# Kernel optimization log

Measured on AMD Instinct MI355X. Metric: run time of the kernel, lower is better.

Reference implementation:

```python
import jax, jax.numpy as jnp
import numpy as np

N_LAYERS = 3
EMB_DIM = 64
N_MASHUP = 100000
N_API = 50000
N_EDGES_MASHUP = 3200000
N_EDGES_API = 1600000
EPS = 1e-12  # F.normalize clamp_min epsilon


def setup_inputs() -> dict:
    key = jax.random.key(0)
    ks = jax.random.split(key, 8)
    return {
        "adj_mashup_rows": jax.random.randint(ks[0], (N_EDGES_MASHUP,), 0, N_MASHUP, dtype=jnp.int32),
        "adj_mashup_cols": jax.random.randint(ks[1], (N_EDGES_MASHUP,), 0, N_MASHUP, dtype=jnp.int32),
        "adj_mashup_vals": jax.random.uniform(ks[2], (N_EDGES_MASHUP,), dtype=jnp.float32),
        "adj_api_rows": jax.random.randint(ks[3], (N_EDGES_API,), 0, N_API, dtype=jnp.int32),
        "adj_api_cols": jax.random.randint(ks[4], (N_EDGES_API,), 0, N_API, dtype=jnp.int32),
        "adj_api_vals": jax.random.uniform(ks[5], (N_EDGES_API,), dtype=jnp.float32),
        "mashup_emb": jax.random.normal(ks[6], (N_MASHUP, EMB_DIM), dtype=jnp.float32),
        "api_emb": jax.random.normal(ks[7], (N_API, EMB_DIM), dtype=jnp.float32),
    }


def _spmm(rows, cols, vals, x, n_nodes):
    # sparse [n,n] @ dense [n,d] via gather + weighted segment-sum
    return jax.ops.segment_sum(vals[:, None] * x[cols], rows, num_segments=n_nodes)


def _propagate(rows, cols, vals, emb):
    n = emb.shape[0]
    acc = emb
    cur = emb
    for _ in range(N_LAYERS):
        cur = _spmm(rows, cols, vals, cur, n)
        acc = acc + cur
    out = acc / (N_LAYERS + 1)  # mean over stacked layers (incl. layer 0)
    norm = jnp.maximum(jnp.linalg.norm(out, axis=1, keepdims=True), EPS)
    return out / norm


def reference(adj_mashup_rows, adj_mashup_cols, adj_mashup_vals,
              adj_api_rows, adj_api_cols, adj_api_vals,
              mashup_emb, api_emb):
    final_mashup = _propagate(adj_mashup_rows, adj_mashup_cols, adj_mashup_vals, mashup_emb)
    final_api = _propagate(adj_api_rows, adj_api_cols, adj_api_vals, api_emb)
    return final_mashup, final_api
```

## Files before the change

kernel.cpp:

```cpp
#include <hip/hip_runtime.h>


#define EMB_DIM 64
#define UNR 8
typedef unsigned long long ull;
typedef int v4i __attribute__((ext_vector_type(4)));

static inline int cdiv(long long a, long long b) { return (int)((a + b - 1) / b); }


__global__ void k_zero2(int* __restrict__ pm, int nm_, int* __restrict__ pa,
                        int na_) {
    int i = blockIdx.x * blockDim.x + threadIdx.x;
    if (i < nm_) pm[i] = 0;
    else if (i < nm_ + na_) pa[i - nm_] = 0;
}

__global__ void k_hist2(const int* __restrict__ rm, int nem,
                        int* __restrict__ posm, const int* __restrict__ ra,
                        int nea, int* __restrict__ posa) {
    int nm4 = nem >> 2, na4 = nea >> 2;
    int i = blockIdx.x * blockDim.x + threadIdx.x;
    if (i < nm4) {
        v4i r = __builtin_nontemporal_load((const v4i*)rm + i);
        atomicAdd(&posm[r.x], 1);
        atomicAdd(&posm[r.y], 1);
        atomicAdd(&posm[r.z], 1);
        atomicAdd(&posm[r.w], 1);
    } else if (i < nm4 + na4) {
        v4i r = __builtin_nontemporal_load((const v4i*)ra + (i - nm4));
        atomicAdd(&posa[r.x], 1);
        atomicAdd(&posa[r.y], 1);
        atomicAdd(&posa[r.z], 1);
        atomicAdd(&posa[r.w], 1);
    } else if (i == nm4 + na4) {
        for (int t = nm4 << 2; t < nem; ++t) atomicAdd(&posm[rm[t]], 1);
        for (int t = na4 << 2; t < nea; ++t) atomicAdd(&posa[ra[t]], 1);
    }
}

#define SCAN_B 256
#define SCAN_E 1024
__global__ void k_scan1(const int* __restrict__ in, int n,
                        int* __restrict__ out, int* __restrict__ bsums) {
    __shared__ int lds[SCAN_B];
    int t = threadIdx.x;
    int base = blockIdx.x * SCAN_E + t * 4;
    int v[4];
    int s = 0;
#pragma unroll
    for (int j = 0; j < 4; ++j) {
        v[j] = (base + j < n) ? in[base + j] : 0;
        s += v[j];
    }
    lds[t] = s;
    __syncthreads();
    for (int off = 1; off < SCAN_B; off <<= 1) {
        int x = (t >= off) ? lds[t - off] : 0;
        __syncthreads();
        lds[t] += x;
        __syncthreads();
    }
    int run = lds[t] - s;
    if (t == SCAN_B - 1) bsums[blockIdx.x] = lds[t];
#pragma unroll
    for (int j = 0; j < 4; ++j) {
        if (base + j < n) out[base + j] = run;
        run += v[j];
    }
}

__global__ void k_scan2(int* __restrict__ bsums, int nb) {
    __shared__ int lds[1024];
    int t = threadIdx.x;
    int v = (t < nb) ? bsums[t] : 0;
    lds[t] = v;
    __syncthreads();
    for (int off = 1; off < 1024; off <<= 1) {
        int x = (t >= off) ? lds[t - off] : 0;
        __syncthreads();
        lds[t] += x;
        __syncthreads();
    }
    if (t < nb) bsums[t] = lds[t] - v;
}

__global__ void k_scan3(int* __restrict__ row_ptr, int* __restrict__ row_pos,
                        const int* __restrict__ bsums, int n, int ne) {
    int i = blockIdx.x * blockDim.x + threadIdx.x;
    if (i < n) {
        int p = row_ptr[i] + bsums[i >> 10];
        row_ptr[i] = p;
        row_pos[i] = p;
    }
    if (i == 0) row_ptr[n] = ne;
}

__global__ void k_scatter2(const int* __restrict__ rm,
                           const int* __restrict__ cm,
                           const float* __restrict__ vm, int nem,
                           unsigned pmulm, int* __restrict__ posm,
                           ull* __restrict__ evm, const int* __restrict__ ra,
                           const int* __restrict__ ca,
                           const float* __restrict__ va, int nea,
                           unsigned pmula, int* __restrict__ posa,
                           ull* __restrict__ eva, int bm) {
    const int p = blockIdx.x & 7;
    const bool is_m = (int)blockIdx.x < bm;
    const int b = is_m ? blockIdx.x : blockIdx.x - bm;
    const int nslot = (is_m ? bm : (int)gridDim.x - bm) >> 3;
    const int bslot = b >> 3;

    const int* rows = is_m ? rm : ra;
    const int* cols = is_m ? cm : ca;
    const float* vals = is_m ? vm : va;
    const int ne = is_m ? nem : nea;
    const unsigned pmul = is_m ? pmulm : pmula;
    int* row_pos = is_m ? posm : posa;
    ull* ev = is_m ? evm : eva;

    const int nb4 = ne >> 2;
    const v4i* rows4 = (const v4i*)rows;

    for (int g = bslot * blockDim.x + threadIdx.x; g < nb4;
         g += nslot * blockDim.x) {
        v4i r4 = __builtin_nontemporal_load(rows4 + g);
        int base = g << 2;
#pragma unroll
        for (int k = 0; k < 4; ++k) {
            int r = (k == 0) ? r4.x : (k == 1) ? r4.y : (k == 2) ? r4.z : r4.w;
            if ((int)(((unsigned)r * pmul) >> 16) == p) {
                int i = base + k;
                float v = __builtin_nontemporal_load(vals + i);
                int c = __builtin_nontemporal_load(cols + i);
                ull pk = ((ull)__float_as_uint(v) << 32) | (unsigned)c;
                int pos = atomicAdd(&row_pos[r], 1);
                ev[pos] = pk;
            }
        }
    }
    if (bslot == 0 && threadIdx.x == 0) {
        for (int i = nb4 << 2; i < ne; ++i) {
            int r = rows[i];
            if ((int)(((unsigned)r * pmul) >> 16) == p) {
                ull pk = ((ull)__float_as_uint(vals[i]) << 32) |
                         (unsigned)cols[i];
                int pos = atomicAdd(&row_pos[r], 1);
                ev[pos] = pk;
            }
        }
    }
}


__global__ void k_tohalf(const float* __restrict__ s, _Float16* __restrict__ d,
                         int n) {
    int i = (blockIdx.x * blockDim.x + threadIdx.x) * 4;
    if (i < n) {
        float4 v = *reinterpret_cast<const float4*>(s + i);
        _Float16 h[4] = {(_Float16)v.x, (_Float16)v.y, (_Float16)v.z,
                         (_Float16)v.w};
        *reinterpret_cast<ushort4*>(d + i) = *reinterpret_cast<ushort4*>(h);
    }
}

template <bool FIRST, bool LAST>
__global__ void k_spmm_quad(const ull* __restrict__ ev,
                            const int* __restrict__ row_ptr,
                            const _Float16* __restrict__ x,
                            _Float16* __restrict__ nxt,
                            float* __restrict__ acc,
                            const float* __restrict__ emb, int nrows) {
    int row = (int)((blockIdx.x * blockDim.x + threadIdx.x) >> 6);
    if (row >= nrows) return;
    int lane = threadIdx.x & 63;
    int q = lane >> 4;
    int sub = lane & 15;

    int s = row_ptr[row];
    int cnt = row_ptr[row + 1] - s;
    const ull* evr = ev + s;

    float a0[UNR], a1[UNR], a2[UNR], a3[UNR];
#pragma unroll
    for (int k = 0; k < UNR; ++k) {
        a0[k] = 0.f; a1[k] = 0.f; a2[k] = 0.f; a3[k] = 0.f;
    }

    int j = 0;
    for (; j + 4 * UNR <= cnt; j += 4 * UNR) {
        ull p[UNR];
#pragma unroll
        for (int k = 0; k < UNR; ++k)
            p[k] = __builtin_nontemporal_load(evr + j + 4 * k + q);
#pragma unroll
        for (int k = 0; k < UNR; ++k) {
            unsigned c = (unsigned)p[k];
            ull xd = *reinterpret_cast<const ull*>(
                x + ((size_t)c << 6) + (sub << 2));
            float v = __uint_as_float((unsigned)(p[k] >> 32));
            union { ull u; _Float16 f[4]; } cv;
            cv.u = xd;
            a0[k] = fmaf(v, (float)cv.f[0], a0[k]);
            a1[k] = fmaf(v, (float)cv.f[1], a1[k]);
            a2[k] = fmaf(v, (float)cv.f[2], a2[k]);
            a3[k] = fmaf(v, (float)cv.f[3], a3[k]);
        }
    }
    if (j < cnt) {
        ull p[UNR];
        bool act[UNR];
#pragma unroll
        for (int k = 0; k < UNR; ++k) {
            int slot = j + 4 * k + q;
            act[k] = slot < cnt;
            p[k] = act[k] ? __builtin_nontemporal_load(evr + slot) : 0ull;
        }
#pragma unroll
        for (int k = 0; k < UNR; ++k) {
            if (act[k]) {
                unsigned c = (unsigned)p[k];
                ull xd = *reinterpret_cast<const ull*>(
                    x + ((size_t)c << 6) + (sub << 2));
                float v = __uint_as_float((unsigned)(p[k] >> 32));
                union { ull u; _Float16 f[4]; } cv;
                cv.u = xd;
                a0[k] = fmaf(v, (float)cv.f[0], a0[k]);
                a1[k] = fmaf(v, (float)cv.f[1], a1[k]);
                a2[k] = fmaf(v, (float)cv.f[2], a2[k]);
                a3[k] = fmaf(v, (float)cv.f[3], a3[k]);
            }
        }
    }
    float t0 = 0.f, t1 = 0.f, t2 = 0.f, t3 = 0.f;
#pragma unroll
    for (int k = 0; k < UNR; ++k) {
        t0 += a0[k]; t1 += a1[k]; t2 += a2[k]; t3 += a3[k];
    }
    t0 += __shfl_xor(t0, 16); t0 += __shfl_xor(t0, 32);
    t1 += __shfl_xor(t1, 16); t1 += __shfl_xor(t1, 32);
    t2 += __shfl_xor(t2, 16); t2 += __shfl_xor(t2, 32);
    t3 += __shfl_xor(t3, 16); t3 += __shfl_xor(t3, 32);

    size_t base = ((size_t)row << 6) + (sub << 2);
    if (FIRST || !LAST) {
        if (q == 0) {
            float4 prev;
            if (FIRST)
                prev = *reinterpret_cast<const float4*>(emb + base);
            else
                prev = *reinterpret_cast<const float4*>(acc + base);
            float4 o = make_float4(prev.x + t0, prev.y + t1, prev.z + t2,
                                   prev.w + t3);
            *reinterpret_cast<float4*>(acc + base) = o;
            union { _Float16 f[4]; ull u; } h;
            h.f[0] = (_Float16)t0; h.f[1] = (_Float16)t1;
            h.f[2] = (_Float16)t2; h.f[3] = (_Float16)t3;
            *reinterpret_cast<ull*>(nxt + base) = h.u;
        }
    } else {
        float4 a2v = *reinterpret_cast<const float4*>(acc + base);
        float b0 = (a2v.x + t0) * 0.25f;
        float b1 = (a2v.y + t1) * 0.25f;
        float b2 = (a2v.z + t2) * 0.25f;
        float b3 = (a2v.w + t3) * 0.25f;
        float ss = b0 * b0 + b1 * b1 + b2 * b2 + b3 * b3;
#pragma unroll
        for (int off = 8; off; off >>= 1) ss += __shfl_xor(ss, off);
        float nrm = fmaxf(sqrtf(ss), 1e-12f);
        if (q == 0) {
            float4 o = make_float4(b0 / nrm, b1 / nrm, b2 / nrm, b3 / nrm);
            *reinterpret_cast<float4*>(acc + base) = o;
        }
    }
}


__global__ void k_copy2(const float4* __restrict__ src, float4* __restrict__ a,
                        float4* __restrict__ b, int n4) {
    int i = blockIdx.x * blockDim.x + threadIdx.x;
    if (i < n4) {
        float4 v = src[i];
        a[i] = v;
        b[i] = v;
    }
}

__global__ void k_zero(float4* __restrict__ p, int n4) {
    int i = blockIdx.x * blockDim.x + threadIdx.x;
    if (i < n4) p[i] = make_float4(0.f, 0.f, 0.f, 0.f);
}

__global__ void k_axpy(float4* __restrict__ acc, const float4* __restrict__ x,
                       int n4) {
    int i = blockIdx.x * blockDim.x + threadIdx.x;
    if (i < n4) {
        float4 a = acc[i];
        float4 v = x[i];
        a.x += v.x; a.y += v.y; a.z += v.z; a.w += v.w;
        acc[i] = a;
    }
}

__global__ void k_spmm_atomic(const int* __restrict__ rows,
                              const int* __restrict__ cols,
                              const float* __restrict__ vals,
                              const float* __restrict__ x,
                              float* __restrict__ y, int n_edges) {
    unsigned tid = blockIdx.x * blockDim.x + threadIdx.x;
    unsigned e = tid >> 4;
    if (e >= (unsigned)n_edges) return;
    int sub = tid & 15;
    int r = rows[e];
    int c = cols[e];
    float v = vals[e];
    const float4 xv =
        *reinterpret_cast<const float4*>(x + ((size_t)c << 6) + (sub << 2));
    float* yp = y + ((size_t)r << 6) + (sub << 2);
    unsafeAtomicAdd(yp + 0, v * xv.x);
    unsafeAtomicAdd(yp + 1, v * xv.y);
    unsafeAtomicAdd(yp + 2, v * xv.z);
    unsafeAtomicAdd(yp + 3, v * xv.w);
}

__global__ void k_normalize(float* __restrict__ out, int nrows) {
    int row = blockIdx.x * 4 + (threadIdx.x >> 6);
    if (row >= nrows) return;
    int lane = threadIdx.x & 63;
    size_t idx = ((size_t)row << 6) + lane;
    float v = out[idx] * 0.25f;
    float s = v * v;
#pragma unroll
    for (int off = 32; off; off >>= 1) s += __shfl_xor(s, off);
    float norm = fmaxf(sqrtf(s), 1e-12f);
    out[idx] = v / norm;
}


extern "C" void kernel_launch(void* const* d_in, const int* in_sizes, int n_in,
                              void* d_out, int out_size, void* d_ws,
                              size_t ws_size, hipStream_t stream) {
    const int* m_rows = (const int*)d_in[0];
    const int* m_cols = (const int*)d_in[1];
    const float* m_vals = (const float*)d_in[2];
    const int* a_rows = (const int*)d_in[3];
    const int* a_cols = (const int*)d_in[4];
    const float* a_vals = (const float*)d_in[5];
    const float* m_emb = (const float*)d_in[6];
    const float* a_emb = (const float*)d_in[7];

    int ne_m = in_sizes[0];
    int ne_a = in_sizes[3];
    int nm = in_sizes[6] / EMB_DIM;
    int na = in_sizes[7] / EMB_DIM;

    size_t elems_m = (size_t)nm * EMB_DIM;
    int nmax = nm > na ? nm : na;
    float* out_m = (float*)d_out;
    float* out_a = out_m + elems_m;

    char* w = (char*)d_ws;
    ull* ev_m = (ull*)w;            w += (size_t)ne_m * sizeof(ull);
    ull* ev_a = (ull*)w;            w += (size_t)ne_a * sizeof(ull);
    _Float16* x0h = (_Float16*)w;   w += (size_t)nmax * EMB_DIM * sizeof(_Float16);
    _Float16* buf0h = (_Float16*)w; w += (size_t)nmax * EMB_DIM * sizeof(_Float16);
    int* row_ptr_m = (int*)w;       w += ((size_t)nm + 1) * sizeof(int);
    int* row_pos_m = (int*)w;       w += (size_t)nm * sizeof(int);
    int* row_ptr_a = (int*)w;       w += ((size_t)na + 1) * sizeof(int);
    int* row_pos_a = (int*)w;       w += (size_t)na * sizeof(int);
    int* bsums = (int*)w;           w += 1024 * sizeof(int);
    size_t need = (size_t)(w - (char*)d_ws);

    if (ws_size >= need) {
        k_zero2<<<cdiv(nm + na, 256), 256, 0, stream>>>(row_pos_m, nm,
                                                        row_pos_a, na);
        k_hist2<<<cdiv((ne_m >> 2) + (ne_a >> 2) + 1, 256), 256, 0, stream>>>(
            m_rows, ne_m, row_pos_m, a_rows, ne_a, row_pos_a);
        int nsb_m = cdiv(nm, SCAN_E);
        k_scan1<<<nsb_m, SCAN_B, 0, stream>>>(row_pos_m, nm, row_ptr_m, bsums);
        k_scan2<<<1, 1024, 0, stream>>>(bsums, nsb_m);
        k_scan3<<<cdiv(nm, 256), 256, 0, stream>>>(row_ptr_m, row_pos_m, bsums,
                                                   nm, ne_m);
        int nsb_a = cdiv(na, SCAN_E);
        k_scan1<<<nsb_a, SCAN_B, 0, stream>>>(row_pos_a, na, row_ptr_a, bsums);
        k_scan2<<<1, 1024, 0, stream>>>(bsums, nsb_a);
        k_scan3<<<cdiv(na, 256), 256, 0, stream>>>(row_ptr_a, row_pos_a, bsums,
                                                   na, ne_a);
        unsigned pmul_m = (unsigned)(((unsigned long long)8 << 16) / (unsigned)nm);
        unsigned pmul_a = (unsigned)(((unsigned long long)8 << 16) / (unsigned)na);
        k_scatter2<<<2048, 256, 0, stream>>>(m_rows, m_cols, m_vals, ne_m,
                                             pmul_m, row_pos_m, ev_m, a_rows,
                                             a_cols, a_vals, ne_a, pmul_a,
                                             row_pos_a, ev_a, 1408);

        auto run_spmm = [&](ull* ev, int* row_ptr, const float* emb,
                            float* out, int n) {
            int nel = n * EMB_DIM;
            k_tohalf<<<cdiv(nel / 4, 256), 256, 0, stream>>>(emb, x0h, nel);
            int g = cdiv(n, 4);
            k_spmm_quad<true, false><<<g, 256, 0, stream>>>(
                ev, row_ptr, x0h, buf0h, out, emb, n);
            k_spmm_quad<false, false><<<g, 256, 0, stream>>>(
                ev, row_ptr, buf0h, x0h, out, nullptr, n);
            k_spmm_quad<false, true><<<g, 256, 0, stream>>>(
                ev, row_ptr, x0h, nullptr, out, nullptr, n);
        };
        run_spmm(ev_m, row_ptr_m, m_emb, out_m, nm);
        run_spmm(ev_a, row_ptr_a, a_emb, out_a, na);
        return;
    }

    float* fb0 = (float*)d_ws;
    float* fb1 = fb0 + elems_m;
    auto run_atomic = [&](const int* rows, const int* cols, const float* vals,
                          const float* emb, float* out, int nrows,
                          int nedges) {
        size_t n = (size_t)nrows * EMB_DIM;
        int n4 = (int)(n / 4);
        int eg = cdiv(n4, 256);
        k_copy2<<<eg, 256, 0, stream>>>((const float4*)emb, (float4*)out,
                                        (float4*)fb0, n4);
        float* cur = fb0;
        float* nxt = fb1;
        int spmm_grid = cdiv((long long)nedges * 16, 256);
        for (int l = 0; l < 3; ++l) {
            k_zero<<<eg, 256, 0, stream>>>((float4*)nxt, n4);
            k_spmm_atomic<<<spmm_grid, 256, 0, stream>>>(rows, cols, vals, cur,
                                                         nxt, nedges);
            k_axpy<<<eg, 256, 0, stream>>>((float4*)out, (const float4*)nxt,
                                           n4);
            float* t = cur; cur = nxt; nxt = t;
        }
        k_normalize<<<cdiv(nrows, 4), 256, 0, stream>>>(out, nrows);
    };
    run_atomic(m_rows, m_cols, m_vals, m_emb, out_m, nm, ne_m);
    run_atomic(a_rows, a_cols, a_vals, a_emb, out_a, na, ne_a);
}
```

Before: 969.9 us.

## Bucket CSR edges within each row by column range for gather locality

The CSR build now counts and scatters edges by a (row, column-chunk) key instead of by row alone, so edges inside each row are grouped by column range, with chunks sized so each chunk's fp16 embeddings span about 2 MB. The aim is more cache locality in the x[cols] gathers of the three SpMM passes. The key counters and scan block sums are placed in the fp16 ping-pong buffer, which frees the separate row_pos arrays. The cost is a larger histogram and scan (NC times more keys), an extra read of the column array in the histogram, and a dependence on that aliasing fitting in the buffer.

```diff
diff --git a/kernel.cpp b/kernel.cpp
--- a/kernel.cpp
+++ b/kernel.cpp
@@ -9,33 +9,39 @@
 static inline int cdiv(long long a, long long b) { return (int)((a + b - 1) / b); }
 
 
-__global__ void k_zero2(int* __restrict__ pm, int nm_, int* __restrict__ pa,
-                        int na_) {
-    int i = blockIdx.x * blockDim.x + threadIdx.x;
-    if (i < nm_) pm[i] = 0;
-    else if (i < nm_ + na_) pa[i - nm_] = 0;
-}
-
-__global__ void k_hist2(const int* __restrict__ rm, int nem,
-                        int* __restrict__ posm, const int* __restrict__ ra,
-                        int nea, int* __restrict__ posa) {
+__global__ void k_zero_i(int* __restrict__ p, int n) {
+    int i = blockIdx.x * blockDim.x + threadIdx.x;
+    if (i < n) p[i] = 0;
+}
+
+__global__ void k_histk2(const int* __restrict__ rm, const int* __restrict__ cm,
+                         int nem, int NCm, unsigned cmulm, int* __restrict__ km,
+                         const int* __restrict__ ra, const int* __restrict__ ca,
+                         int nea, int NCa, unsigned cmula, int* __restrict__ ka) {
     int nm4 = nem >> 2, na4 = nea >> 2;
     int i = blockIdx.x * blockDim.x + threadIdx.x;
     if (i < nm4) {
         v4i r = __builtin_nontemporal_load((const v4i*)rm + i);
-        atomicAdd(&posm[r.x], 1);
-        atomicAdd(&posm[r.y], 1);
-        atomicAdd(&posm[r.z], 1);
-        atomicAdd(&posm[r.w], 1);
+        v4i c = __builtin_nontemporal_load((const v4i*)cm + i);
+        atomicAdd(&km[r.x * NCm + (int)(((unsigned)c.x * cmulm) >> 16)], 1);
+        atomicAdd(&km[r.y * NCm + (int)(((unsigned)c.y * cmulm) >> 16)], 1);
+        atomicAdd(&km[r.z * NCm + (int)(((unsigned)c.z * cmulm) >> 16)], 1);
+        atomicAdd(&km[r.w * NCm + (int)(((unsigned)c.w * cmulm) >> 16)], 1);
     } else if (i < nm4 + na4) {
-        v4i r = __builtin_nontemporal_load((const v4i*)ra + (i - nm4));
-        atomicAdd(&posa[r.x], 1);
-        atomicAdd(&posa[r.y], 1);
-        atomicAdd(&posa[r.z], 1);
-        atomicAdd(&posa[r.w], 1);
+        int ii = i - nm4;
+        v4i r = __builtin_nontemporal_load((const v4i*)ra + ii);
+        v4i c = __builtin_nontemporal_load((const v4i*)ca + ii);
+        atomicAdd(&ka[r.x * NCa + (int)(((unsigned)c.x * cmula) >> 16)], 1);
+        atomicAdd(&ka[r.y * NCa + (int)(((unsigned)c.y * cmula) >> 16)], 1);
+        atomicAdd(&ka[r.z * NCa + (int)(((unsigned)c.z * cmula) >> 16)], 1);
+        atomicAdd(&ka[r.w * NCa + (int)(((unsigned)c.w * cmula) >> 16)], 1);
     } else if (i == nm4 + na4) {
-        for (int t = nm4 << 2; t < nem; ++t) atomicAdd(&posm[rm[t]], 1);
-        for (int t = na4 << 2; t < nea; ++t) atomicAdd(&posa[ra[t]], 1);
+        for (int t = nm4 << 2; t < nem; ++t)
+            atomicAdd(&km[rm[t] * NCm +
+                          (int)(((unsigned)cm[t] * cmulm) >> 16)], 1);
+        for (int t = na4 << 2; t < nea; ++t)
+            atomicAdd(&ka[ra[t] * NCa +
+                          (int)(((unsigned)ca[t] * cmula) >> 16)], 1);
     }
 }
 
@@ -85,26 +91,29 @@
     if (t < nb) bsums[t] = lds[t] - v;
 }
 
-__global__ void k_scan3(int* __restrict__ row_ptr, int* __restrict__ row_pos,
-                        const int* __restrict__ bsums, int n, int ne) {
-    int i = blockIdx.x * blockDim.x + threadIdx.x;
-    if (i < n) {
-        int p = row_ptr[i] + bsums[i >> 10];
-        row_ptr[i] = p;
-        row_pos[i] = p;
-    }
-    if (i == 0) row_ptr[n] = ne;
-}
-
-__global__ void k_scatter2(const int* __restrict__ rm,
-                           const int* __restrict__ cm,
-                           const float* __restrict__ vm, int nem,
-                           unsigned pmulm, int* __restrict__ posm,
-                           ull* __restrict__ evm, const int* __restrict__ ra,
-                           const int* __restrict__ ca,
-                           const float* __restrict__ va, int nea,
-                           unsigned pmula, int* __restrict__ posa,
-                           ull* __restrict__ eva, int bm) {
+__global__ void k_scan3b(int* __restrict__ kpos, const int* __restrict__ bsums,
+                         int nk, int ne, int NC, int* __restrict__ row_ptr,
+                         int nrows) {
+    int i = blockIdx.x * blockDim.x + threadIdx.x;
+    if (i < nk) {
+        int p = kpos[i] + bsums[i >> 10];
+        kpos[i] = p;
+        if (i % NC == 0) row_ptr[i / NC] = p;
+    }
+    if (i == 0) row_ptr[nrows] = ne;
+}
+
+__global__ void k_scatterk2(const int* __restrict__ rm,
+                            const int* __restrict__ cm,
+                            const float* __restrict__ vm, int nem,
+                            unsigned pmulm, int NCm, unsigned cmulm,
+                            int* __restrict__ km, ull* __restrict__ evm,
+                            const int* __restrict__ ra,
+                            const int* __restrict__ ca,
+                            const float* __restrict__ va, int nea,
+                            unsigned pmula, int NCa, unsigned cmula,
+                            int* __restrict__ ka, ull* __restrict__ eva,
+                            int bm) {
     const int p = blockIdx.x & 7;
     const bool is_m = (int)blockIdx.x < bm;
     const int b = is_m ? blockIdx.x : blockIdx.x - bm;
@@ -116,7 +125,9 @@
     const float* vals = is_m ? vm : va;
     const int ne = is_m ? nem : nea;
     const unsigned pmul = is_m ? pmulm : pmula;
-    int* row_pos = is_m ? posm : posa;
+    const int NC = is_m ? NCm : NCa;
+    const unsigned cmul = is_m ? cmulm : cmula;
+    int* kpos = is_m ? km : ka;
     ull* ev = is_m ? evm : eva;
 
     const int nb4 = ne >> 2;
@@ -133,8 +144,9 @@
                 int i = base + k;
                 float v = __builtin_nontemporal_load(vals + i);
                 int c = __builtin_nontemporal_load(cols + i);
+                int key = r * NC + (int)(((unsigned)c * cmul) >> 16);
                 ull pk = ((ull)__float_as_uint(v) << 32) | (unsigned)c;
-                int pos = atomicAdd(&row_pos[r], 1);
+                int pos = atomicAdd(&kpos[key], 1);
                 ev[pos] = pk;
             }
         }
@@ -143,9 +155,10 @@
         for (int i = nb4 << 2; i < ne; ++i) {
             int r = rows[i];
             if ((int)(((unsigned)r * pmul) >> 16) == p) {
-                ull pk = ((ull)__float_as_uint(vals[i]) << 32) |
-                         (unsigned)cols[i];
-                int pos = atomicAdd(&row_pos[r], 1);
+                int c = cols[i];
+                int key = r * NC + (int)(((unsigned)c * cmul) >> 16);
+                ull pk = ((ull)__float_as_uint(vals[i]) << 32) | (unsigned)c;
+                int pos = atomicAdd(&kpos[key], 1);
                 ev[pos] = pk;
             }
         }
@@ -359,39 +372,55 @@
     float* out_m = (float*)d_out;
     float* out_a = out_m + elems_m;
 
+    int NC_m = cdiv((long long)nm * 2 * EMB_DIM, 2097152);
+    int NC_a = cdiv((long long)na * 2 * EMB_DIM, 2097152);
+    if (NC_m < 1) NC_m = 1;
+    if (NC_a < 1) NC_a = 1;
+    int nk_m = nm * NC_m;
+    int nk_a = na * NC_a;
+
     char* w = (char*)d_ws;
     ull* ev_m = (ull*)w;            w += (size_t)ne_m * sizeof(ull);
     ull* ev_a = (ull*)w;            w += (size_t)ne_a * sizeof(ull);
     _Float16* x0h = (_Float16*)w;   w += (size_t)nmax * EMB_DIM * sizeof(_Float16);
     _Float16* buf0h = (_Float16*)w; w += (size_t)nmax * EMB_DIM * sizeof(_Float16);
     int* row_ptr_m = (int*)w;       w += ((size_t)nm + 1) * sizeof(int);
-    int* row_pos_m = (int*)w;       w += (size_t)nm * sizeof(int);
     int* row_ptr_a = (int*)w;       w += ((size_t)na + 1) * sizeof(int);
-    int* row_pos_a = (int*)w;       w += (size_t)na * sizeof(int);
-    int* bsums = (int*)w;           w += 1024 * sizeof(int);
     size_t need = (size_t)(w - (char*)d_ws);
 
-    if (ws_size >= need) {
-        k_zero2<<<cdiv(nm + na, 256), 256, 0, stream>>>(row_pos_m, nm,
-                                                        row_pos_a, na);
-        k_hist2<<<cdiv((ne_m >> 2) + (ne_a >> 2) + 1, 256), 256, 0, stream>>>(
-            m_rows, ne_m, row_pos_m, a_rows, ne_a, row_pos_a);
-        int nsb_m = cdiv(nm, SCAN_E);
-        k_scan1<<<nsb_m, SCAN_B, 0, stream>>>(row_pos_m, nm, row_ptr_m, bsums);
-        k_scan2<<<1, 1024, 0, stream>>>(bsums, nsb_m);
-        k_scan3<<<cdiv(nm, 256), 256, 0, stream>>>(row_ptr_m, row_pos_m, bsums,
-                                                   nm, ne_m);
-        int nsb_a = cdiv(na, SCAN_E);
-        k_scan1<<<nsb_a, SCAN_B, 0, stream>>>(row_pos_a, na, row_ptr_a, bsums);
-        k_scan2<<<1, 1024, 0, stream>>>(bsums, nsb_a);
-        k_scan3<<<cdiv(na, 256), 256, 0, stream>>>(row_ptr_a, row_pos_a, bsums,
-                                                   na, ne_a);
+    int* kpos_m = (int*)buf0h;
+    int* kpos_a = kpos_m + nk_m;
+    int* bsums = kpos_a + nk_a;
+    bool alias_ok =
+        ((size_t)nk_m + nk_a + 1024) * sizeof(int) <= (size_t)nmax * EMB_DIM * 2;
+
+    if (ws_size >= need && alias_ok) {
+        unsigned cmul_m = (unsigned)(((unsigned long long)NC_m << 16) / (unsigned)nm);
+        unsigned cmul_a = (unsigned)(((unsigned long long)NC_a << 16) / (unsigned)na);
         unsigned pmul_m = (unsigned)(((unsigned long long)8 << 16) / (unsigned)nm);
         unsigned pmul_a = (unsigned)(((unsigned long long)8 << 16) / (unsigned)na);
-        k_scatter2<<<2048, 256, 0, stream>>>(m_rows, m_cols, m_vals, ne_m,
-                                             pmul_m, row_pos_m, ev_m, a_rows,
-                                             a_cols, a_vals, ne_a, pmul_a,
-                                             row_pos_a, ev_a, 1408);
+
+        k_zero_i<<<cdiv(nk_m + nk_a, 256), 256, 0, stream>>>(kpos_m,
+                                                             nk_m + nk_a);
+        k_histk2<<<cdiv((ne_m >> 2) + (ne_a >> 2) + 1, 256), 256, 0, stream>>>(
+            m_rows, m_cols, ne_m, NC_m, cmul_m, kpos_m, a_rows, a_cols, ne_a,
+            NC_a, cmul_a, kpos_a);
+        int nsb_m = cdiv(nk_m, SCAN_E);
+        k_scan1<<<nsb_m, SCAN_B, 0, stream>>>(kpos_m, nk_m, kpos_m, bsums);
+        k_scan2<<<1, 1024, 0, stream>>>(bsums, nsb_m);
+        k_scan3b<<<cdiv(nk_m, 256), 256, 0, stream>>>(kpos_m, bsums, nk_m,
+                                                      ne_m, NC_m, row_ptr_m,
+                                                      nm);
+        int nsb_a = cdiv(nk_a, SCAN_E);
+        k_scan1<<<nsb_a, SCAN_B, 0, stream>>>(kpos_a, nk_a, kpos_a, bsums);
+        k_scan2<<<1, 1024, 0, stream>>>(bsums, nsb_a);
+        k_scan3b<<<cdiv(nk_a, 256), 256, 0, stream>>>(kpos_a, bsums, nk_a,
+                                                      ne_a, NC_a, row_ptr_a,
+                                                      na);
+        k_scatterk2<<<2048, 256, 0, stream>>>(
+            m_rows, m_cols, m_vals, ne_m, pmul_m, NC_m, cmul_m, kpos_m, ev_m,
+            a_rows, a_cols, a_vals, ne_a, pmul_a, NC_a, cmul_a, kpos_a, ev_a,
+            1408);
 
         auto run_spmm = [&](ull* ev, int* row_ptr, const float* emb,
                             float* out, int n) {
```

After: 985.4 us. About the same (+1.6%).

## Merge mashup and API pipelines into shared launches and alias scratch buffers

Applied to the files above, without the earlier changes.

Fuses the scan, fp16 conversion and three SpMM layer kernels for the mashup and API graphs into single launches that dispatch by block or wave index. This cuts kernel launch count and lets the smaller API graph fill the GPU alongside the mashup graph instead of running serially. Row-position counters and block sums are aliased onto the fp16 embedding buffer to save workspace, and each graph now has its own fp16 buffers. The aliasing relies on the scatter finishing before the tohalf conversion overwrites that memory.

```diff
diff --git a/kernel.cpp b/kernel.cpp
--- a/kernel.cpp
+++ b/kernel.cpp
@@ -41,11 +41,21 @@
 
 #define SCAN_B 256
 #define SCAN_E 1024
-__global__ void k_scan1(const int* __restrict__ in, int n,
-                        int* __restrict__ out, int* __restrict__ bsums) {
+
+__global__ void k_scan1m(const int* __restrict__ inm, int nm_,
+                         int* __restrict__ outm, int* __restrict__ bsm,
+                         int nsbm, const int* __restrict__ ina, int na_,
+                         int* __restrict__ outa, int* __restrict__ bsa) {
+    bool is_m = (int)blockIdx.x < nsbm;
+    const int* in = is_m ? inm : ina;
+    int* out = is_m ? outm : outa;
+    int* bsums = is_m ? bsm : bsa;
+    int n = is_m ? nm_ : na_;
+    int b = is_m ? blockIdx.x : blockIdx.x - nsbm;
+
     __shared__ int lds[SCAN_B];
     int t = threadIdx.x;
-    int base = blockIdx.x * SCAN_E + t * 4;
+    int base = b * SCAN_E + t * 4;
     int v[4];
     int s = 0;
 #pragma unroll
@@ -62,7 +72,7 @@
         __syncthreads();
     }
     int run = lds[t] - s;
-    if (t == SCAN_B - 1) bsums[blockIdx.x] = lds[t];
+    if (t == SCAN_B - 1) bsums[b] = lds[t];
 #pragma unroll
     for (int j = 0; j < 4; ++j) {
         if (base + j < n) out[base + j] = run;
@@ -70,7 +80,10 @@
     }
 }
 
-__global__ void k_scan2(int* __restrict__ bsums, int nb) {
+__global__ void k_scan2m(int* __restrict__ bsm, int nbm, int* __restrict__ bsa,
+                         int nba) {
+    int* bsums = (blockIdx.x == 0) ? bsm : bsa;
+    int nb = (blockIdx.x == 0) ? nbm : nba;
     __shared__ int lds[1024];
     int t = threadIdx.x;
     int v = (t < nb) ? bsums[t] : 0;
@@ -85,15 +98,23 @@
     if (t < nb) bsums[t] = lds[t] - v;
 }
 
-__global__ void k_scan3(int* __restrict__ row_ptr, int* __restrict__ row_pos,
-                        const int* __restrict__ bsums, int n, int ne) {
-    int i = blockIdx.x * blockDim.x + threadIdx.x;
-    if (i < n) {
-        int p = row_ptr[i] + bsums[i >> 10];
-        row_ptr[i] = p;
-        row_pos[i] = p;
-    }
-    if (i == 0) row_ptr[n] = ne;
+__global__ void k_scan3m(int* __restrict__ rpm, int* __restrict__ posm,
+                         const int* __restrict__ bsm, int nm_, int nem,
+                         int* __restrict__ rpa, int* __restrict__ posa,
+                         const int* __restrict__ bsa, int na_, int nea) {
+    int i = blockIdx.x * blockDim.x + threadIdx.x;
+    if (i < nm_) {
+        int p = rpm[i] + bsm[i >> 10];
+        rpm[i] = p;
+        posm[i] = p;
+        if (i == 0) rpm[nm_] = nem;
+    } else if (i < nm_ + na_) {
+        int ii = i - nm_;
+        int p = rpa[ii] + bsa[ii >> 10];
+        rpa[ii] = p;
+        posa[ii] = p;
+        if (ii == 0) rpa[na_] = nea;
+    }
 }
 
 __global__ void k_scatter2(const int* __restrict__ rm,
@@ -153,27 +174,34 @@
 }
 
 
-__global__ void k_tohalf(const float* __restrict__ s, _Float16* __restrict__ d,
-                         int n) {
-    int i = (blockIdx.x * blockDim.x + threadIdx.x) * 4;
-    if (i < n) {
-        float4 v = *reinterpret_cast<const float4*>(s + i);
-        _Float16 h[4] = {(_Float16)v.x, (_Float16)v.y, (_Float16)v.z,
-                         (_Float16)v.w};
-        *reinterpret_cast<ushort4*>(d + i) = *reinterpret_cast<ushort4*>(h);
-    }
+__global__ void k_tohalf2(const float* __restrict__ sm, _Float16* __restrict__ dm,
+                          int nm4, const float* __restrict__ sa,
+                          _Float16* __restrict__ da, int na4) {
+    int i = blockIdx.x * blockDim.x + threadIdx.x;
+    const float* s;
+    _Float16* d;
+    int j;
+    if (i < nm4) {
+        s = sm; d = dm; j = i;
+    } else if (i < nm4 + na4) {
+        s = sa; d = da; j = i - nm4;
+    } else {
+        return;
+    }
+    float4 v = *reinterpret_cast<const float4*>(s + j * 4);
+    _Float16 h[4] = {(_Float16)v.x, (_Float16)v.y, (_Float16)v.z,
+                     (_Float16)v.w};
+    *reinterpret_cast<ushort4*>(d + j * 4) = *reinterpret_cast<ushort4*>(h);
 }
 
 template <bool FIRST, bool LAST>
-__global__ void k_spmm_quad(const ull* __restrict__ ev,
-                            const int* __restrict__ row_ptr,
-                            const _Float16* __restrict__ x,
-                            _Float16* __restrict__ nxt,
-                            float* __restrict__ acc,
-                            const float* __restrict__ emb, int nrows) {
-    int row = (int)((blockIdx.x * blockDim.x + threadIdx.x) >> 6);
-    if (row >= nrows) return;
-    int lane = threadIdx.x & 63;
+__device__ __forceinline__ void spmm_row(const ull* __restrict__ ev,
+                                         const int* __restrict__ row_ptr,
+                                         const _Float16* __restrict__ x,
+                                         _Float16* __restrict__ nxt,
+                                         float* __restrict__ acc,
+                                         const float* __restrict__ emb,
+                                         int row, int lane) {
     int q = lane >> 4;
     int sub = lane & 15;
 
@@ -272,6 +300,26 @@
             float4 o = make_float4(b0 / nrm, b1 / nrm, b2 / nrm, b3 / nrm);
             *reinterpret_cast<float4*>(acc + base) = o;
         }
+    }
+}
+
+template <bool FIRST, bool LAST>
+__global__ void k_spmm2(const ull* __restrict__ evm,
+                        const int* __restrict__ rpm,
+                        const _Float16* __restrict__ xm,
+                        _Float16* __restrict__ nxm, float* __restrict__ accm,
+                        const float* __restrict__ embm, int nm_,
+                        const ull* __restrict__ eva,
+                        const int* __restrict__ rpa,
+                        const _Float16* __restrict__ xa,
+                        _Float16* __restrict__ nxa, float* __restrict__ acca,
+                        const float* __restrict__ emba, int na_) {
+    int wid = (int)((blockIdx.x * blockDim.x + threadIdx.x) >> 6);
+    int lane = threadIdx.x & 63;
+    if (wid < nm_) {
+        spmm_row<FIRST, LAST>(evm, rpm, xm, nxm, accm, embm, wid, lane);
+    } else if (wid < nm_ + na_) {
+        spmm_row<FIRST, LAST>(eva, rpa, xa, nxa, acca, emba, wid - nm_, lane);
     }
 }
 
@@ -355,58 +403,61 @@
     int na = in_sizes[7] / EMB_DIM;
 
     size_t elems_m = (size_t)nm * EMB_DIM;
-    int nmax = nm > na ? nm : na;
+    size_t elems_a = (size_t)na * EMB_DIM;
     float* out_m = (float*)d_out;
     float* out_a = out_m + elems_m;
 
     char* w = (char*)d_ws;
     ull* ev_m = (ull*)w;            w += (size_t)ne_m * sizeof(ull);
     ull* ev_a = (ull*)w;            w += (size_t)ne_a * sizeof(ull);
-    _Float16* x0h = (_Float16*)w;   w += (size_t)nmax * EMB_DIM * sizeof(_Float16);
-    _Float16* buf0h = (_Float16*)w; w += (size_t)nmax * EMB_DIM * sizeof(_Float16);
+    _Float16* x0h_m = (_Float16*)w; w += elems_m * sizeof(_Float16);
+    _Float16* buf_m = (_Float16*)w; w += elems_m * sizeof(_Float16);
+    _Float16* x0h_a = (_Float16*)w; w += elems_a * sizeof(_Float16);
+    _Float16* buf_a = (_Float16*)w; w += elems_a * sizeof(_Float16);
     int* row_ptr_m = (int*)w;       w += ((size_t)nm + 1) * sizeof(int);
-    int* row_pos_m = (int*)w;       w += (size_t)nm * sizeof(int);
     int* row_ptr_a = (int*)w;       w += ((size_t)na + 1) * sizeof(int);
-    int* row_pos_a = (int*)w;       w += (size_t)na * sizeof(int);
-    int* bsums = (int*)w;           w += 1024 * sizeof(int);
     size_t need = (size_t)(w - (char*)d_ws);
 
-    if (ws_size >= need) {
+    int* row_pos_m = (int*)x0h_m;
+    int* row_pos_a = row_pos_m + nm;
+    int* bsums_m = row_pos_a + na;
+    int* bsums_a = bsums_m + 1024;
+    bool alias_ok = ((size_t)nm + na + 2048) * sizeof(int) <=
+                    elems_m * sizeof(_Float16);
+
+    if (ws_size >= need && alias_ok) {
         k_zero2<<<cdiv(nm + na, 256), 256, 0, stream>>>(row_pos_m, nm,
                                                         row_pos_a, na);
         k_hist2<<<cdiv((ne_m >> 2) + (ne_a >> 2) + 1, 256), 256, 0, stream>>>(
             m_rows, ne_m, row_pos_m, a_rows, ne_a, row_pos_a);
         int nsb_m = cdiv(nm, SCAN_E);
-        k_scan1<<<nsb_m, SCAN_B, 0, stream>>>(row_pos_m, nm, row_ptr_m, bsums);
-        k_scan2<<<1, 1024, 0, stream>>>(bsums, nsb_m);
-        k_scan3<<<cdiv(nm, 256), 256, 0, stream>>>(row_ptr_m, row_pos_m, bsums,
-                                                   nm, ne_m);
         int nsb_a = cdiv(na, SCAN_E);
-        k_scan1<<<nsb_a, SCAN_B, 0, stream>>>(row_pos_a, na, row_ptr_a, bsums);
-        k_scan2<<<1, 1024, 0, stream>>>(bsums, nsb_a);
-        k_scan3<<<cdiv(na, 256), 256, 0, stream>>>(row_ptr_a, row_pos_a, bsums,
-                                                   na, ne_a);
+        k_scan1m<<<nsb_m + nsb_a, SCAN_B, 0, stream>>>(
+            row_pos_m, nm, row_ptr_m, bsums_m, nsb_m, row_pos_a, na,
+            row_ptr_a, bsums_a);
+        k_scan2m<<<2, 1024, 0, stream>>>(bsums_m, nsb_m, bsums_a, nsb_a);
+        k_scan3m<<<cdiv(nm + na, 256), 256, 0, stream>>>(
+            row_ptr_m, row_pos_m, bsums_m, nm, ne_m, row_ptr_a, row_pos_a,
+            bsums_a, na, ne_a);
         unsigned pmul_m = (unsigned)(((unsigned long long)8 << 16) / (unsigned)nm);
         unsigned pmul_a = (unsigned)(((unsigned long long)8 << 16) / (unsigned)na);
         k_scatter2<<<2048, 256, 0, stream>>>(m_rows, m_cols, m_vals, ne_m,
                                              pmul_m, row_pos_m, ev_m, a_rows,
                                              a_cols, a_vals, ne_a, pmul_a,
                                              row_pos_a, ev_a, 1408);
-
-        auto run_spmm = [&](ull* ev, int* row_ptr, const float* emb,
-                            float* out, int n) {
-            int nel = n * EMB_DIM;
-            k_tohalf<<<cdiv(nel / 4, 256), 256, 0, stream>>>(emb, x0h, nel);
-            int g = cdiv(n, 4);
-            k_spmm_quad<true, false><<<g, 256, 0, stream>>>(
-                ev, row_ptr, x0h, buf0h, out, emb, n);
-            k_spmm_quad<false, false><<<g, 256, 0, stream>>>(
-                ev, row_ptr, buf0h, x0h, out, nullptr, n);
-            k_spmm_quad<false, true><<<g, 256, 0, stream>>>(
-                ev, row_ptr, x0h, nullptr, out, nullptr, n);
-        };
-        run_spmm(ev_m, row_ptr_m, m_emb, out_m, nm);
-        run_spmm(ev_a, row_ptr_a, a_emb, out_a, na);
+        int nm4 = (int)(elems_m / 4), na4 = (int)(elems_a / 4);
+        k_tohalf2<<<cdiv(nm4 + na4, 256), 256, 0, stream>>>(
+            m_emb, x0h_m, nm4, a_emb, x0h_a, na4);
+        int g = cdiv(nm + na, 4);
+        k_spmm2<true, false><<<g, 256, 0, stream>>>(
+            ev_m, row_ptr_m, x0h_m, buf_m, out_m, m_emb, nm,
+            ev_a, row_ptr_a, x0h_a, buf_a, out_a, a_emb, na);
+        k_spmm2<false, false><<<g, 256, 0, stream>>>(
+            ev_m, row_ptr_m, buf_m, x0h_m, out_m, nullptr, nm,
+            ev_a, row_ptr_a, buf_a, x0h_a, out_a, nullptr, na);
+        k_spmm2<false, true><<<g, 256, 0, stream>>>(
+            ev_m, row_ptr_m, x0h_m, nullptr, out_m, nullptr, nm,
+            ev_a, row_ptr_a, x0h_a, nullptr, out_a, nullptr, na);
         return;
     }
 
```

Result: faster. 950.8 us (-2.0%).
